# Kernel tuning notes

Measured on AMD Instinct MI355X. Metric: run time of the kernel, lower is better.

Reference implementation:

```python
import jax, jax.numpy as jnp
import numpy as np

N_LAGS = 64
EPS = 1e-8


def setup_inputs() -> dict:
    key = jax.random.key(0)
    x = jax.random.normal(key, (16, 8, 250, 1024), dtype=jnp.float32)
    return {"x": x}


def reference(x):
    B, M, T, L = x.shape
    # rfft over all mics once (shared across pairs)
    X = jnp.fft.rfft(x, axis=-1)  # [B, M, T, L//2+1] complex
    # all mic pairs (m1 < m2), row-major order matching the torch double loop
    i1, i2 = np.triu_indices(M, k=1)
    X1 = X[:, i1]  # [B, P, T, F]
    X2 = X[:, i2]  # [B, P, T, F]
    R = X1 * jnp.conj(X2)
    R = R / (jnp.abs(R) + EPS)  # PHAT weighting
    cc = jnp.fft.irfft(R, n=L, axis=-1)        # [B, P, T, L]
    cc = jnp.fft.fftshift(cc, axes=-1)
    center = L // 2
    start = center - N_LAGS // 2
    return cc[..., start:start + N_LAGS]        # [B, P, T, n_lags]
```

## Files before the change

### kernel.cpp

```cpp
#include <hip/hip_runtime.h>
#include <math.h>

#define B_    16
#define M_    8
#define T_    250
#define L_    1024
#define NPAIR 28

#define KTOT   1024
#define CH_K   256
#define NKT    8
#define NCHUNK 4
#define APITCH 264
#define XPLANE (516 * 8)

typedef _Float16 half8  __attribute__((ext_vector_type(8)));
typedef _Float16 half2t __attribute__((ext_vector_type(2)));
typedef float    floatx4 __attribute__((ext_vector_type(4)));

__device__ __align__(16) _Float16 g_Btw[64 * KTOT];

__constant__ int c_i1[NPAIR] = {0,0,0,0,0,0,0,1,1,1,1,1,1,2,2,2,2,2,3,3,3,3,4,4,4,5,5,6};
__constant__ int c_i2[NPAIR] = {1,2,3,4,5,6,7,2,3,4,5,6,7,3,4,5,6,7,4,5,6,7,5,6,7,6,7,7};

__global__ void init_btw() {
    int idx = blockIdx.x * 256 + threadIdx.x;
    int n = idx >> 10, k = idx & 1023;
    float v;
    if (k == 0)      v = 1.0f / 1024.0f;
    else if (k == 1) v = (n & 1) ? (-1.0f / 1024.0f) : (1.0f / 1024.0f);
    else {
        int bin = k >> 1, tau = n - 32;
        int r = (tau * bin) & 1023;
        float ang = (float)r * (6.283185307179586f / 1024.0f);
        float s, c; sincosf(ang, &s, &c);
        v = ((k & 1) ? -s : c) * (2.0f / 1024.0f);
    }
    g_Btw[idx] = (_Float16)v;
}

#define PHI(i) ((i) ^ (((i) >> 4) & 15) ^ ((((i) >> 8) & 3) << 1))

__device__ inline float2 cmul(float2 a, float2 b) {
    return make_float2(fmaf(a.x, b.x, -a.y * b.y), fmaf(a.x, b.y, a.y * b.x));
}
__device__ inline float2 cadd(float2 a, float2 b) { return make_float2(a.x + b.x, a.y + b.y); }
__device__ inline float2 csub(float2 a, float2 b) { return make_float2(a.x - b.x, a.y - b.y); }
__device__ inline float2 cmni(float2 a) { return make_float2(a.y, -a.x); }

__device__ inline void dft8(float2 v[8]) {
    const float rt = 0.70710678118654752440f;
    float2 b0 = cadd(v[0], v[4]), b1 = cadd(v[1], v[5]);
    float2 b2 = cadd(v[2], v[6]), b3 = cadd(v[3], v[7]);
    float2 c0 = csub(v[0], v[4]);
    float2 t1 = csub(v[1], v[5]);
    float2 c1 = make_float2(rt * (t1.x + t1.y), rt * (t1.y - t1.x));
    float2 c2 = cmni(csub(v[2], v[6]));
    float2 t3 = csub(v[3], v[7]);
    float2 c3 = make_float2(rt * (t3.y - t3.x), -rt * (t3.x + t3.y));
    float2 f0 = cadd(b0, b2), f1 = cadd(b1, b3);
    float2 g0 = csub(b0, b2), g1 = cmni(csub(b1, b3));
    v[0] = cadd(f0, f1); v[4] = csub(f0, f1);
    v[2] = cadd(g0, g1); v[6] = csub(g0, g1);
    f0 = cadd(c0, c2); f1 = cadd(c1, c3);
    g0 = csub(c0, c2); g1 = cmni(csub(c1, c3));
    v[1] = cadd(f0, f1); v[5] = csub(f0, f1);
    v[3] = cadd(g0, g1); v[7] = csub(g0, g1);
}

__device__ inline void twiddle8(float2 v[8], float2 w1) {
    float2 w2 = cmul(w1, w1);
    float2 w3 = cmul(w2, w1);
    float2 w4 = cmul(w2, w2);
    float2 w5 = cmul(w4, w1);
    float2 w6 = cmul(w4, w2);
    float2 w7 = cmul(w4, w3);
    v[1] = cmul(v[1], w1); v[2] = cmul(v[2], w2); v[3] = cmul(v[3], w3);
    v[4] = cmul(v[4], w4); v[5] = cmul(v[5], w5); v[6] = cmul(v[6], w6);
    v[7] = cmul(v[7], w7);
}

__device__ inline int posmap(int k) {
    return ((k & 1) << 9) | (((k >> 1) & 7) << 6) | (((k >> 4) & 7) << 3) | ((k >> 7) & 7);
}

union SMem {
    float2 z[4 * 1024];
    struct {
        _Float16 X[2 * XPLANE];
        _Float16 A[32 * APITCH];
    } p;
};

__global__ __launch_bounds__(512, 4) void gcc_main(const float* __restrict__ x,
                                                   float* __restrict__ out) {
    __shared__ __align__(16) SMem sm;

    const int tid = threadIdx.x;
    const int t = blockIdx.x, b = blockIdx.y;
    const int f = tid & 127, c = tid >> 7;
    char* Zc = (char*)(sm.z + c * 1024);

    float ws, wc;
    sincosf((float)f * (-6.283185307179586f / 1024.0f), &ws, &wc);
    const float2 w = make_float2(wc, ws);

    {
        const float* xa = x + (((size_t)b * M_ + 2 * c) * T_ + t) * L_;
        const float* xb = xa + (size_t)T_ * L_;
        float va[8], vb[8];
#pragma unroll
        for (int j = 0; j < 8; ++j) { va[j] = xa[f + 128 * j]; vb[j] = xb[f + 128 * j]; }
        const int KR8 = (f ^ ((f >> 4) & 7)) * 8;
        const float rt = 0.70710678118654752440f;
#pragma unroll
        for (int q = 0; q < 4; ++q) {
            float2 a = make_float2(va[q], vb[q]);
            float2 d = make_float2(va[q + 4], vb[q + 4]);
            float2 tq = cmul(csub(a, d), w);
            float2 r;
            if (q == 0)      r = tq;
            else if (q == 1) r = make_float2(rt * (tq.x + tq.y), rt * (tq.y - tq.x));
            else if (q == 2) r = make_float2(tq.y, -tq.x);
            else             r = make_float2(rt * (tq.y - tq.x), -rt * (tq.x + tq.y));
            const int E1 = ((q << 7) ^ ((q & 1) << 3) ^ ((q >> 1) << 1)) * 8;
            const int E2 = E1 ^ (512 * 8) ^ (4 * 8);
            *(float2*)(Zc + (KR8 ^ E1)) = cadd(a, d);
            *(float2*)(Zc + (KR8 ^ E2)) = r;
        }
    }
    __syncthreads();

    {
        float2 wl = w;
        if (f & 64) wl = cmul(wl, make_float2(0.92387953251128674f, 0.38268343236508977f));
        const float2 wB = cmul(wl, wl);
        const int u = f & 63, s9 = f >> 6;
        const int KB8 = (((s9 << 9) + u) ^ (u >> 4) ^ (s9 << 2)) * 8;
        float2 v[8];
#pragma unroll
        for (int r = 0; r < 8; ++r)
            v[r] = *(const float2*)(Zc + (KB8 ^ (((r << 6) | ((r & 3) << 2) | ((r >> 2) << 1)) * 8)));
        dft8(v);
        twiddle8(v, wB);
#pragma unroll
        for (int k = 0; k < 8; ++k)
            *(float2*)(Zc + (KB8 ^ (((k << 6) | ((k & 3) << 2) | ((k >> 2) << 1)) * 8))) = v[k];
    }
    __syncthreads();

    {
        float s2, c2;
        sincosf((float)(f & 7) * (-6.283185307179586f / 64.0f), &s2, &c2);
        const float2 wC = make_float2(c2, s2);
        const int g = f >> 3, v3 = f & 7;
        const int KC8 = (((g << 6) + v3) ^ ((g & 3) << 2) ^ (((g >> 2) & 3) << 1)) * 8;
        float2 v[8];
#pragma unroll
        for (int r = 0; r < 8; ++r)
            v[r] = *(const float2*)(Zc + (KC8 ^ (((r << 3) | ((r >> 1) & 3)) * 8)));
        dft8(v);
        twiddle8(v, wC);
#pragma unroll
        for (int k = 0; k < 8; ++k)
            *(float2*)(Zc + (KC8 ^ (((k << 3) | ((k >> 1) & 3)) * 8))) = v[k];
    }
    __syncthreads();

    {
        const int KD8 = ((f << 3) ^ ((f >> 1) & 15) ^ (((f >> 5) & 3) << 1)) * 8;
        float2 v[8];
#pragma unroll
        for (int r = 0; r < 8; ++r)
            v[r] = *(const float2*)(Zc + (KD8 ^ (r * 8)));
        dft8(v);
#pragma unroll
        for (int k = 0; k < 8; ++k)
            *(float2*)(Zc + (KD8 ^ (k * 8))) = v[k];
    }
    __syncthreads();

    {
        const int k = tid;
        const int pa = PHI(posmap(k));
        const int pb = PHI(posmap((1024 - k) & 1023));
        float2 Z8[8];
#pragma unroll
        for (int cc = 0; cc < 4; ++cc) {
            Z8[2 * cc]     = sm.z[cc * 1024 + pa];
            Z8[2 * cc + 1] = sm.z[cc * 1024 + pb];
        }
        float2 ny0 = make_float2(0.f, 0.f), ny1 = ny0, ny2 = ny0, ny3 = ny0;
        if (tid == 0) {
            ny0 = sm.z[0 * 1024 + 4]; ny1 = sm.z[1 * 1024 + 4];
            ny2 = sm.z[2 * 1024 + 4]; ny3 = sm.z[3 * 1024 + 4];
        }
        __syncthreads();

        half8 lo, hi;
#pragma unroll
        for (int cc = 0; cc < 4; ++cc) {
            float2 Aa = Z8[2 * cc], Bb = Z8[2 * cc + 1];
            float xr = Aa.x + Bb.x, xi = Aa.y - Bb.y;
            float yr = Aa.y + Bb.y, yi = Bb.x - Aa.x;
            float mx = fmaf(xr, xr, xi * xi);
            float ix = (mx > 1e-30f) ? rsqrtf(mx) : 0.0f;
            float my = fmaf(yr, yr, yi * yi);
            float iy = (my > 1e-30f) ? rsqrtf(my) : 0.0f;
            xr *= ix; xi *= ix; yr *= iy; yi *= iy;
            const int o = (cc & 1) * 4;
            if (cc < 2) {
                lo[o + 0] = (_Float16)xr; lo[o + 1] = (_Float16)xi;
                lo[o + 2] = (_Float16)yr; lo[o + 3] = (_Float16)yi;
            } else {
                hi[o + 0] = (_Float16)xr; hi[o + 1] = (_Float16)xi;
                hi[o + 2] = (_Float16)yr; hi[o + 3] = (_Float16)yi;
            }
        }
        *(half8*)(sm.p.X + 0 * XPLANE + k * 8) = lo;
        *(half8*)(sm.p.X + 1 * XPLANE + k * 8) = hi;
        if (tid == 0) {
            half8 nlo, nhi;
#define SGN(s_) ((_Float16)(((s_) * (s_) > 1e-30f) ? copysignf(1.0f, (s_)) : 0.0f))
            nlo[0] = SGN(ny0.x); nlo[1] = (_Float16)0.f;
            nlo[2] = SGN(ny0.y); nlo[3] = (_Float16)0.f;
            nlo[4] = SGN(ny1.x); nlo[5] = (_Float16)0.f;
            nlo[6] = SGN(ny1.y); nlo[7] = (_Float16)0.f;
            nhi[0] = SGN(ny2.x); nhi[1] = (_Float16)0.f;
            nhi[2] = SGN(ny2.y); nhi[3] = (_Float16)0.f;
            nhi[4] = SGN(ny3.x); nhi[5] = (_Float16)0.f;
            nhi[6] = SGN(ny3.y); nhi[7] = (_Float16)0.f;
#undef SGN
            *(half8*)(sm.p.X + 0 * XPLANE + 512 * 8) = nlo;
            *(half8*)(sm.p.X + 1 * XPLANE + 512 * 8) = nhi;
        }
        __syncthreads();
    }

    const int lane = tid & 63, wv = tid >> 6;
    const int mt = wv >> 2, nt = wv & 3;
    const int l15 = lane & 15, quad = lane >> 4;
    const int arow = mt * 16 + l15;
    const _Float16* Bbase = g_Btw + (nt * 16 + l15) * KTOT;
    floatx4 acc = {0.0f, 0.0f, 0.0f, 0.0f};

    const int bl = tid & 127, pg = tid >> 7;

#define PAIRA(p_, a_, b_)                                                     \
    {                                                                         \
        float2 U1 = Xs[a_], U2 = Xs[b_];                                      \
        float rr = fmaf(U1.x, U2.x, U1.y * U2.y);                             \
        float ri = fmaf(U1.y, U2.x, -U1.x * U2.y);                            \
        *(half2t*)&sm.p.A[(p_) * APITCH + 2 * bl] =                           \
            (half2t){(_Float16)rr, (_Float16)ri};                             \
    }

    auto fillA = [&](int h) {
        const int bin = h * 128 + bl;
        half8 lo = *(const half8*)(sm.p.X + 0 * XPLANE + bin * 8);
        half8 hi = *(const half8*)(sm.p.X + 1 * XPLANE + bin * 8);
        float2 Xs[8];
#pragma unroll
        for (int ch = 0; ch < 4; ++ch) {
            Xs[ch]     = make_float2((float)lo[2 * ch], (float)lo[2 * ch + 1]);
            Xs[4 + ch] = make_float2((float)hi[2 * ch], (float)hi[2 * ch + 1]);
        }
        if (pg == 0) {
            PAIRA(0, 0, 1) PAIRA(1, 0, 2) PAIRA(2, 0, 3) PAIRA(3, 0, 4)
            PAIRA(4, 0, 5) PAIRA(5, 0, 6) PAIRA(6, 0, 7)
        } else if (pg == 1) {
            PAIRA(7, 1, 2) PAIRA(8, 1, 3) PAIRA(9, 1, 4) PAIRA(10, 1, 5)
            PAIRA(11, 1, 6) PAIRA(12, 1, 7) PAIRA(13, 2, 3)
        } else if (pg == 2) {
            PAIRA(14, 2, 4) PAIRA(15, 2, 5) PAIRA(16, 2, 6) PAIRA(17, 2, 7)
            PAIRA(18, 3, 4) PAIRA(19, 3, 5) PAIRA(20, 3, 6)
        } else {
            PAIRA(21, 3, 7) PAIRA(22, 4, 5) PAIRA(23, 4, 6) PAIRA(24, 4, 7)
            PAIRA(25, 5, 6) PAIRA(26, 5, 7) PAIRA(27, 6, 7)
        }
        if (h == 0 && bl == 0) {
#pragma unroll
            for (int pp = 0; pp < 7; ++pp) {
                const int p = pg * 7 + pp;
                const int ca = c_i1[p], cb = c_i2[p];
                float x1 = (float)sm.p.X[(ca >> 2) * XPLANE + 512 * 8 + (ca & 3) * 2];
                float x2 = (float)sm.p.X[(cb >> 2) * XPLANE + 512 * 8 + (cb & 3) * 2];
                sm.p.A[p * APITCH + 1] = (_Float16)(x1 * x2);
            }
        }
    };

    for (int h = 0; h < NCHUNK; ++h) {
        fillA(h);
        __syncthreads();

        const _Float16* Ap = sm.p.A + arow * APITCH;
        const _Float16* Bp = Bbase + h * CH_K;
#pragma unroll
        for (int kt = 0; kt < NKT; ++kt) {
            half8 af = *(const half8*)(Ap + kt * 32 + quad * 8);
            half8 bf = *(const half8*)(Bp + kt * 32 + quad * 8);
            acc = __builtin_amdgcn_mfma_f32_16x16x32_f16(af, bf, acc, 0, 0, 0);
        }
        __syncthreads();
    }

#pragma unroll
    for (int r = 0; r < 4; ++r) {
        int pair = mt * 16 + quad * 4 + r;
        if (pair < NPAIR)
            out[((((size_t)b * NPAIR + pair) * T_ + t) << 6) + nt * 16 + l15] = acc[r];
    }
}

extern "C" void kernel_launch(void* const* d_in, const int* in_sizes, int n_in,
                              void* d_out, int out_size, void* d_ws, size_t ws_size,
                              hipStream_t stream) {
    (void)in_sizes; (void)n_in; (void)d_ws; (void)ws_size; (void)out_size;
    hipLaunchKernelGGL(init_btw, dim3(256), dim3(256), 0, stream);
    hipLaunchKernelGGL(gcc_main, dim3(T_, B_), dim3(512), 0, stream,
                       (const float*)d_in[0], (float*)d_out);
}
```

Baseline: 287.8 us.

## Compute cross-spectrum MFMA operands in registers directly from per-channel spectra

```diff
diff --git a/kernel.cpp b/kernel.cpp
--- a/kernel.cpp
+++ b/kernel.cpp
@@ -8,11 +8,7 @@
 #define NPAIR 28
 
 #define KTOT   1024
-#define CH_K   256
-#define NKT    8
-#define NCHUNK 4
-#define APITCH 264
-#define XPLANE (516 * 8)
+#define XTS    516
 
 typedef _Float16 half8  __attribute__((ext_vector_type(8)));
 typedef _Float16 half2t __attribute__((ext_vector_type(2)));
@@ -20,8 +16,8 @@
 
 __device__ __align__(16) _Float16 g_Btw[64 * KTOT];
 
-__constant__ int c_i1[NPAIR] = {0,0,0,0,0,0,0,1,1,1,1,1,1,2,2,2,2,2,3,3,3,3,4,4,4,5,5,6};
-__constant__ int c_i2[NPAIR] = {1,2,3,4,5,6,7,2,3,4,5,6,7,3,4,5,6,7,4,5,6,7,5,6,7,6,7,7};
+__constant__ int c_i1x[32] = {0,0,0,0,0,0,0,1,1,1,1,1,1,2,2,2,2,2,3,3,3,3,4,4,4,5,5,6, 0,0,0,0};
+__constant__ int c_i2x[32] = {1,2,3,4,5,6,7,2,3,4,5,6,7,3,4,5,6,7,4,5,6,7,5,6,7,6,7,7, 0,0,0,0};
 
 __global__ void init_btw() {
     int idx = blockIdx.x * 256 + threadIdx.x;
@@ -86,10 +82,7 @@
 
 union SMem {
     float2 z[4 * 1024];
-    struct {
-        _Float16 X[2 * XPLANE];
-        _Float16 A[32 * APITCH];
-    } p;
+    half2t X[8 * XTS];
 };
 
 __global__ __launch_bounds__(512, 4) void gcc_main(const float* __restrict__ x,
@@ -197,7 +190,6 @@
         }
         __syncthreads();
 
-        half8 lo, hi;
 #pragma unroll
         for (int cc = 0; cc < 4; ++cc) {
             float2 Aa = Z8[2 * cc], Bb = Z8[2 * cc + 1];
@@ -207,32 +199,20 @@
             float ix = (mx > 1e-30f) ? rsqrtf(mx) : 0.0f;
             float my = fmaf(yr, yr, yi * yi);
             float iy = (my > 1e-30f) ? rsqrtf(my) : 0.0f;
-            xr *= ix; xi *= ix; yr *= iy; yi *= iy;
-            const int o = (cc & 1) * 4;
-            if (cc < 2) {
-                lo[o + 0] = (_Float16)xr; lo[o + 1] = (_Float16)xi;
-                lo[o + 2] = (_Float16)yr; lo[o + 3] = (_Float16)yi;
-            } else {
-                hi[o + 0] = (_Float16)xr; hi[o + 1] = (_Float16)xi;
-                hi[o + 2] = (_Float16)yr; hi[o + 3] = (_Float16)yi;
-            }
-        }
-        *(half8*)(sm.p.X + 0 * XPLANE + k * 8) = lo;
-        *(half8*)(sm.p.X + 1 * XPLANE + k * 8) = hi;
+            sm.X[(2 * cc) * XTS + k]     = (half2t){(_Float16)(xr * ix), (_Float16)(xi * ix)};
+            sm.X[(2 * cc + 1) * XTS + k] = (half2t){(_Float16)(yr * iy), (_Float16)(yi * iy)};
+        }
         if (tid == 0) {
-            half8 nlo, nhi;
 #define SGN(s_) ((_Float16)(((s_) * (s_) > 1e-30f) ? copysignf(1.0f, (s_)) : 0.0f))
-            nlo[0] = SGN(ny0.x); nlo[1] = (_Float16)0.f;
-            nlo[2] = SGN(ny0.y); nlo[3] = (_Float16)0.f;
-            nlo[4] = SGN(ny1.x); nlo[5] = (_Float16)0.f;
-            nlo[6] = SGN(ny1.y); nlo[7] = (_Float16)0.f;
-            nhi[0] = SGN(ny2.x); nhi[1] = (_Float16)0.f;
-            nhi[2] = SGN(ny2.y); nhi[3] = (_Float16)0.f;
-            nhi[4] = SGN(ny3.x); nhi[5] = (_Float16)0.f;
-            nhi[6] = SGN(ny3.y); nhi[7] = (_Float16)0.f;
+            sm.X[0 * XTS + 512] = (half2t){SGN(ny0.x), (_Float16)0.f};
+            sm.X[1 * XTS + 512] = (half2t){SGN(ny0.y), (_Float16)0.f};
+            sm.X[2 * XTS + 512] = (half2t){SGN(ny1.x), (_Float16)0.f};
+            sm.X[3 * XTS + 512] = (half2t){SGN(ny1.y), (_Float16)0.f};
+            sm.X[4 * XTS + 512] = (half2t){SGN(ny2.x), (_Float16)0.f};
+            sm.X[5 * XTS + 512] = (half2t){SGN(ny2.y), (_Float16)0.f};
+            sm.X[6 * XTS + 512] = (half2t){SGN(ny3.x), (_Float16)0.f};
+            sm.X[7 * XTS + 512] = (half2t){SGN(ny3.y), (_Float16)0.f};
 #undef SGN
-            *(half8*)(sm.p.X + 0 * XPLANE + 512 * 8) = nlo;
-            *(half8*)(sm.p.X + 1 * XPLANE + 512 * 8) = nhi;
         }
         __syncthreads();
     }
@@ -241,68 +221,34 @@
     const int mt = wv >> 2, nt = wv & 3;
     const int l15 = lane & 15, quad = lane >> 4;
     const int arow = mt * 16 + l15;
-    const _Float16* Bbase = g_Btw + (nt * 16 + l15) * KTOT;
+    const half2t* Ua = sm.X + c_i1x[arow] * XTS;
+    const half2t* Ub = sm.X + c_i2x[arow] * XTS;
+    const _Float16* Bp = g_Btw + (nt * 16 + l15) * KTOT + quad * 8;
+    const float nyp = (float)Ua[512][0] * (float)Ub[512][0];
     floatx4 acc = {0.0f, 0.0f, 0.0f, 0.0f};
 
-    const int bl = tid & 127, pg = tid >> 7;
-
-#define PAIRA(p_, a_, b_)                                                     \
-    {                                                                         \
-        float2 U1 = Xs[a_], U2 = Xs[b_];                                      \
-        float rr = fmaf(U1.x, U2.x, U1.y * U2.y);                             \
-        float ri = fmaf(U1.y, U2.x, -U1.x * U2.y);                            \
-        *(half2t*)&sm.p.A[(p_) * APITCH + 2 * bl] =                           \
-            (half2t){(_Float16)rr, (_Float16)ri};                             \
-    }
-
-    auto fillA = [&](int h) {
-        const int bin = h * 128 + bl;
-        half8 lo = *(const half8*)(sm.p.X + 0 * XPLANE + bin * 8);
-        half8 hi = *(const half8*)(sm.p.X + 1 * XPLANE + bin * 8);
-        float2 Xs[8];
-#pragma unroll
-        for (int ch = 0; ch < 4; ++ch) {
-            Xs[ch]     = make_float2((float)lo[2 * ch], (float)lo[2 * ch + 1]);
-            Xs[4 + ch] = make_float2((float)hi[2 * ch], (float)hi[2 * ch + 1]);
-        }
-        if (pg == 0) {
-            PAIRA(0, 0, 1) PAIRA(1, 0, 2) PAIRA(2, 0, 3) PAIRA(3, 0, 4)
-            PAIRA(4, 0, 5) PAIRA(5, 0, 6) PAIRA(6, 0, 7)
-        } else if (pg == 1) {
-            PAIRA(7, 1, 2) PAIRA(8, 1, 3) PAIRA(9, 1, 4) PAIRA(10, 1, 5)
-            PAIRA(11, 1, 6) PAIRA(12, 1, 7) PAIRA(13, 2, 3)
-        } else if (pg == 2) {
-            PAIRA(14, 2, 4) PAIRA(15, 2, 5) PAIRA(16, 2, 6) PAIRA(17, 2, 7)
-            PAIRA(18, 3, 4) PAIRA(19, 3, 5) PAIRA(20, 3, 6)
-        } else {
-            PAIRA(21, 3, 7) PAIRA(22, 4, 5) PAIRA(23, 4, 6) PAIRA(24, 4, 7)
-            PAIRA(25, 5, 6) PAIRA(26, 5, 7) PAIRA(27, 6, 7)
-        }
-        if (h == 0 && bl == 0) {
-#pragma unroll
-            for (int pp = 0; pp < 7; ++pp) {
-                const int p = pg * 7 + pp;
-                const int ca = c_i1[p], cb = c_i2[p];
-                float x1 = (float)sm.p.X[(ca >> 2) * XPLANE + 512 * 8 + (ca & 3) * 2];
-                float x2 = (float)sm.p.X[(cb >> 2) * XPLANE + 512 * 8 + (cb & 3) * 2];
-                sm.p.A[p * APITCH + 1] = (_Float16)(x1 * x2);
+#pragma unroll 1
+    for (int h = 0; h < 4; ++h) {
+        const int hb = h * 128;
+#pragma unroll
+        for (int kt = 0; kt < 8; ++kt) {
+            const int b0 = hb + kt * 16 + quad * 4;
+            half8 ua = *(const half8*)(Ua + b0);
+            half8 ub = *(const half8*)(Ub + b0);
+            half8 af;
+#pragma unroll
+            for (int j = 0; j < 4; ++j) {
+                float ar = (float)ua[2 * j], ai = (float)ua[2 * j + 1];
+                float br = (float)ub[2 * j], bi = (float)ub[2 * j + 1];
+                af[2 * j]     = (_Float16)fmaf(ar, br,  ai * bi);
+                af[2 * j + 1] = (_Float16)fmaf(ai, br, -ar * bi);
             }
-        }
-    };
-
-    for (int h = 0; h < NCHUNK; ++h) {
-        fillA(h);
-        __syncthreads();
-
-        const _Float16* Ap = sm.p.A + arow * APITCH;
-        const _Float16* Bp = Bbase + h * CH_K;
-#pragma unroll
-        for (int kt = 0; kt < NKT; ++kt) {
-            half8 af = *(const half8*)(Ap + kt * 32 + quad * 8);
-            half8 bf = *(const half8*)(Bp + kt * 32 + quad * 8);
+            if (kt == 0) {
+                if (h == 0) af[1] = (quad == 0) ? (_Float16)nyp : af[1];
+            }
+            half8 bf = *(const half8*)(Bp + (h * 8 + kt) * 32);
             acc = __builtin_amdgcn_mfma_f32_16x16x32_f16(af, bf, acc, 0, 0, 0);
         }
-        __syncthreads();
     }
 
 #pragma unroll
```

New measurement: 298.1 us. 3.6% more time.
